# Kernel tuning notes

Measured on AMD Instinct MI355X. Metric: run time of the kernel, lower is better.

The kernel has to match this reference:

```python
import jax, jax.numpy as jnp
import numpy as np

N_ITEMS = 100001  # n_items + 1 (padding idx 0)
D = 128           # item_embedding_dim == hidden_size
P = 3             # purposes
S, B = 100, 256   # seq_len, batch
TAU = 0.1
EPS = 0.01


def setup_inputs() -> dict:
    key = jax.random.key(0)
    ks = jax.random.split(key, 6)
    std = 1.0 / np.sqrt(D)
    seq = jax.random.randint(ks[0], (S, B), 0, N_ITEMS)          # [S, B] item ids
    lens = jax.random.randint(ks[1], (B,), 1, S + 1)             # valid lengths in [1, S]
    emb_table = jax.random.uniform(ks[2], (N_ITEMS, D), minval=-std, maxval=std, dtype=jnp.float32)
    purpose_table = jax.random.uniform(ks[3], (P, D), minval=-std, maxval=std, dtype=jnp.float32)
    x2h_w = jax.random.uniform(ks[4], (P, 3 * D, D), minval=-std, maxval=std, dtype=jnp.float32)  # 3 cells
    h2h_w = jax.random.uniform(ks[5], (P, 3 * D, D), minval=-std, maxval=std, dtype=jnp.float32)
    return {"seq": seq, "lens": lens, "emb_table": emb_table,
            "purpose_table": purpose_table, "x2h_w": x2h_w, "h2h_w": h2h_w}


def _psru_cell(x, h, concen, Wx, Wh):
    # x: [B,D], h: [B,D], concen: [B], Wx/Wh: [3D, D]
    gx = x @ Wx.T                              # [B, 3D]
    gh = h @ Wh.T                              # [B, 3D]
    i_r, i_i, i_n = jnp.split(gx, 3, axis=1)
    h_r, h_i, h_n = jnp.split(gh, 3, axis=1)
    resetgate = jax.nn.sigmoid(i_r + h_r)
    inputgate = jax.nn.sigmoid(i_i + h_i)
    newgate = jnp.tanh(i_n + resetgate * h_n)
    multi = jnp.where(concen >= EPS, concen, 0.0)[:, None] * inputgate
    return h + multi * (newgate - h)


def reference(seq, lens, emb_table, purpose_table, x2h_w, h2h_w):
    # padding_idx = 0
    emb_table = emb_table.at[0].set(0.0)
    # concentration matrix: softmax over purposes of normalized-embedding similarity / tau
    item_n = emb_table / jnp.clip(jnp.linalg.norm(emb_table, axis=1, keepdims=True), 1e-12)
    attr_n = purpose_table / jnp.clip(jnp.linalg.norm(purpose_table, axis=1, keepdims=True), 1e-12)
    g = jax.nn.softmax((item_n @ attr_n.T) / TAU, axis=1)   # [V, P]  (exp/sum == softmax)
    g = g.at[0].set(0.0)

    embs = emb_table[seq]        # [S, B, D]
    g_seq = g[seq]               # [S, B, P]

    h0 = jnp.zeros((P, B, D), emb_table.dtype)

    def step(h, xs):
        x, gq = xs  # x: [B,D], gq: [B,P]
        h_new = jnp.stack([_psru_cell(x, h[p], gq[:, p], x2h_w[p], h2h_w[p]) for p in range(P)])
        return h_new, h_new

    _, hs = jax.lax.scan(step, h0, (embs, g_seq))            # hs: [S, P, B, D]

    # select hidden at last valid step per example: outs[lens-1, arange(B)]
    h_last = hs[lens - 1, :, jnp.arange(B), :]               # [B, P, D]

    # delta_c[b,v] = sum_p g[v,p] * <h_last[b,p], item_n[v]>  (== original VC_cand * item_embs sum)
    logits = sum((h_last[:, p, :] @ item_n.T) * g[None, :, p] for p in range(P))  # [B, V]
    return jax.nn.sigmoid(logits)
```

## Files before the change

### kernel.cpp

```cpp
#include <hip/hip_runtime.h>
#include <hip/hip_bf16.h>
#include <math.h>

#define N_ITEMS 100001
#define DIM 128
#define NP 3
#define SEQ 100
#define NB 256
#define G3 384
#define TAU 0.1f
#define EPS_C 0.01f

#define OFF_G     0
#define OFF_C     300016
#define OFF_WXT   600032
#define OFF_WHT   747488
#define OFF_HLAST 894944
#define OFF_GX    993248
#define WS_FLOATS_PATHA (993248 + 29491200)

typedef float f32x4 __attribute__((ext_vector_type(4)));
typedef short s16x8 __attribute__((ext_vector_type(8)));
typedef unsigned int u32x4 __attribute__((ext_vector_type(4)));
typedef _Float16 f16x8 __attribute__((ext_vector_type(8)));
typedef __fp16 hf16x2 __attribute__((ext_vector_type(2)));

__device__ __forceinline__ float sigmoidf_fast(float x) {
    return __builtin_amdgcn_rcpf(1.f + __builtin_amdgcn_exp2f(-1.4426950408889634f * x));
}
__device__ __forceinline__ float tanhf_fast(float x) {
    return 1.f - 2.f * __builtin_amdgcn_rcpf(1.f + __builtin_amdgcn_exp2f(2.8853900817779268f * x));
}
__device__ __forceinline__ unsigned short f2bf(float x) {
    union { float f; unsigned u; } v; v.f = x;
    unsigned r = v.u + 0x7fffu + ((v.u >> 16) & 1u);
    return (unsigned short)(r >> 16);
}
__device__ __forceinline__ float bf2f(unsigned short h) {
    union { unsigned u; float f; } v; v.u = ((unsigned)h) << 16;
    return v.f;
}
__device__ __forceinline__ f32x4 mfma16(s16x8 a, s16x8 b, f32x4 c) {
    return __builtin_amdgcn_mfma_f32_16x16x32_f16(
        __builtin_bit_cast(f16x8, a), __builtin_bit_cast(f16x8, b), c, 0, 0, 0);
}

__global__ void k_prep_w(const float* __restrict__ x2h, const float* __restrict__ h2h,
                         float* __restrict__ wxT, float* __restrict__ whT) {
    int idx = blockIdx.x * 256 + threadIdx.x;
    if (idx >= NP * DIM * G3) return;
    int j = idx % G3;
    int k = (idx / G3) % DIM;
    int p = idx / (G3 * DIM);
    wxT[idx] = x2h[((size_t)p * G3 + j) * DIM + k];
    whT[idx] = h2h[((size_t)p * G3 + j) * DIM + k];
}

__global__ __launch_bounds__(256) void k_prep_wA(const float* __restrict__ x2h,
                                                 const float* __restrict__ h2h,
                                                 short* __restrict__ wxA_hi,
                                                 short* __restrict__ wxA_lo,
                                                 short* __restrict__ whA_hi,
                                                 short* __restrict__ whA_lo) {
    int e = blockIdx.x * 256 + threadIdx.x;
    if (e >= 2 * NP * 24 * 4 * 64) return;
    int which = (e >= NP * 24 * 4 * 64);
    int f = which ? e - NP * 24 * 4 * 64 : e;
    const float* tab = which ? h2h : x2h;
    short* dh = which ? whA_hi : wxA_hi;
    short* dl = which ? whA_lo : wxA_lo;
    int lane = f & 63;
    int ks = (f >> 6) & 3;
    int mt = (f >> 8) % 24;
    int p  = f / 6144;
    int j = mt * 16 + (lane & 15);
    int d = ks * 32 + (lane >> 4) * 8;
    const float* src = tab + ((size_t)p * G3 + j) * DIM + d;
    short hi[8], lo[8];
#pragma unroll
    for (int u = 0; u < 8; ++u) {
        float x = src[u];
        _Float16 hf = (_Float16)x;
        _Float16 lf = (_Float16)((x - (float)hf) * 2048.f);
        hi[u] = __builtin_bit_cast(short, hf);
        lo[u] = __builtin_bit_cast(short, lf);
    }
    *(s16x8*)(dh + (size_t)f * 8) = *(const s16x8*)hi;
    *(s16x8*)(dl + (size_t)f * 8) = *(const s16x8*)lo;
}

__global__ __launch_bounds__(256) void k_gc(const float* __restrict__ emb,
                                            const float* __restrict__ pt,
                                            float* __restrict__ g, float* __restrict__ c) {
    __shared__ float pt_l[G3];
    __shared__ float ainv[NP];
    int tid = threadIdx.x;
    for (int u = tid; u < G3; u += 256) pt_l[u] = pt[u];
    __syncthreads();
    if (tid < NP) {
        float ss = 0.f;
        for (int k = 0; k < DIM; ++k) { float v = pt_l[tid * DIM + k]; ss += v * v; }
        ainv[tid] = 1.f / fmaxf(sqrtf(ss), 1e-12f);
    }
    __syncthreads();
    int lane = tid & 63, wv = tid >> 6;
    for (int it = 0; it < 8; ++it) {
        int i = blockIdx.x * 32 + wv * 8 + it;
        if (i >= N_ITEMS) continue;
        float a = emb[(size_t)i * DIM + lane];
        float b = emb[(size_t)i * DIM + 64 + lane];
        float ss = a * a + b * b;
        float d0 = a * pt_l[lane]       + b * pt_l[64 + lane];
        float d1 = a * pt_l[128 + lane] + b * pt_l[192 + lane];
        float d2 = a * pt_l[256 + lane] + b * pt_l[320 + lane];
        for (int off = 32; off > 0; off >>= 1) {
            ss += __shfl_down(ss, off);
            d0 += __shfl_down(d0, off);
            d1 += __shfl_down(d1, off);
            d2 += __shfl_down(d2, off);
        }
        if (lane == 0) {
            if (i == 0) {
                g[0] = 0.f; g[1] = 0.f; g[2] = 0.f;
                c[0] = 0.f; c[1] = 0.f; c[2] = 0.f;
            } else {
                float inv = 1.f / fmaxf(sqrtf(ss), 1e-12f);
                float l0 = d0 * ainv[0] * inv * (1.f / TAU);
                float l1 = d1 * ainv[1] * inv * (1.f / TAU);
                float l2 = d2 * ainv[2] * inv * (1.f / TAU);
                float m = fmaxf(l0, fmaxf(l1, l2));
                float e0 = expf(l0 - m), e1 = expf(l1 - m), e2 = expf(l2 - m);
                float is = 1.f / (e0 + e1 + e2);
                float g0 = e0 * is, g1 = e1 * is, g2 = e2 * is;
                g[(size_t)i * 3 + 0] = g0; g[(size_t)i * 3 + 1] = g1; g[(size_t)i * 3 + 2] = g2;
                c[(size_t)i * 3 + 0] = g0 * inv; c[(size_t)i * 3 + 1] = g1 * inv; c[(size_t)i * 3 + 2] = g2 * inv;
            }
        }
    }
}

__global__ __launch_bounds__(512, 2) void k_gx_mfma(const int* __restrict__ seq,
                                                    const float* __restrict__ emb,
                                                    const short* __restrict__ wxA,
                                                    float* __restrict__ gx) {
    int bid = blockIdx.x;
    int t  = bid >> 4;
    int b0 = (bid & 15) * 16;
    int tid = threadIdx.x;
    int lane = tid & 63;
    int w = tid >> 6;
    int n = lane & 15;
    int q = lane >> 4;

    __shared__ int idx_l[16];
    __shared__ __align__(16) unsigned short xF[2048];

    if (tid < 16) idx_l[tid] = seq[t * NB + b0 + tid];
    __syncthreads();

    {
        int tk = tid >> 5, s = tid & 31;
        float4 v = *(const float4*)(emb + (size_t)idx_l[tk] * DIM + s * 4);
        int k = s * 4;
        int ks = k >> 5, km = k & 31;
        int ln = (km >> 3) * 16 + tk;
        int j0 = km & 7;
        int o = ks * 512 + ln * 8 + j0;
        hf16x2 a01 = __builtin_amdgcn_cvt_pkrtz(v.x, v.y);
        hf16x2 a23 = __builtin_amdgcn_cvt_pkrtz(v.z, v.w);
        *(uint2*)(xF + o) = make_uint2(__builtin_bit_cast(unsigned, a01),
                                       __builtin_bit_cast(unsigned, a23));
    }
    __syncthreads();

    s16x8 bf[4];
#pragma unroll
    for (int ks = 0; ks < 4; ++ks)
        bf[ks] = ((const s16x8*)xF)[ks * 64 + lane];

    float* gxt = gx + (size_t)(t * 3) * NB * G3;
#pragma unroll 3
    for (int ji = 0; ji < 9; ++ji) {
        int pid = w + ji * 8;
        int p = pid / 24, mt = pid % 24;
        f32x4 acc = {0.f, 0.f, 0.f, 0.f};
#pragma unroll
        for (int ks = 0; ks < 4; ++ks) {
            size_t ao = ((((size_t)p * 24 + mt) * 4 + ks) * 64 + lane) * 8;
            s16x8 af = *(const s16x8*)(wxA + ao);
            acc = mfma16(af, bf[ks], acc);
        }
        float* o = gxt + ((size_t)p * NB + b0 + n) * G3 + mt * 16 + q * 4;
        *(float4*)o = make_float4(acc[0], acc[1], acc[2], acc[3]);
    }
}

__global__ __launch_bounds__(1024, 4) void k_rnn3(const int* __restrict__ seq,
                                                  const int* __restrict__ lens,
                                                  const float* __restrict__ g,
                                                  const short* __restrict__ whA_hi,
                                                  const float* __restrict__ gx,
                                                  float* __restrict__ hlast) {
    int bid = blockIdx.x;
    int p  = bid / 8;
    int bg = bid % 8;
    int tid = threadIdx.x;
    int tile2 = tid >> 9;
    int tl  = tid & 511;
    int lane = tid & 63;
    int w = tl >> 6;
    int n = lane & 15;
    int q = lane >> 4;
    int d0 = w * 16 + q * 4;
    int b0 = bg * 32 + tile2 * 16;

    __shared__ __align__(16) unsigned short hH[2 * 4096];
    __shared__ __align__(16) unsigned short hL[2 * 4096];
    __shared__ float conc_s[SEQ * 32];

    for (int u = tid; u < 4096; u += 1024) { hH[u] = 0; hL[u] = 0; }

    for (int e = tid; e < SEQ * 32; e += 1024) {
        int t = e >> 5, b = e & 31;
        int ix = seq[t * NB + bg * 32 + b];
        float cc = g[(size_t)ix * 3 + p];
        conc_s[e] = (cc >= EPS_C) ? cc : 0.f;
    }

    s16x8 whF[3][4];
    int mts0 = w, mts1 = 8 + w, mts2 = 16 + w;
#pragma unroll
    for (int ks = 0; ks < 4; ++ks) {
        size_t o0 = ((((size_t)p * 24 + mts0) * 4 + ks) * 64 + lane) * 8;
        size_t o1 = ((((size_t)p * 24 + mts1) * 4 + ks) * 64 + lane) * 8;
        size_t o2 = ((((size_t)p * 24 + mts2) * 4 + ks) * 64 + lane) * 8;
        whF[0][ks] = *(const s16x8*)(whA_hi + o0);
        whF[1][ks] = *(const s16x8*)(whA_hi + o1);
        whF[2][ks] = *(const s16x8*)(whA_hi + o2);
    }

    int len_n = lens[b0 + n];
    float h0 = 0.f, h1 = 0.f, h2 = 0.f, h3 = 0.f;

    int wks = d0 >> 5;
    int km  = d0 & 31;
    int rl  = (km >> 3) * 16 + n;
    int jj0 = km & 7;
    int widx = wks * 512 + rl * 8 + jj0;

    const float* gxbase = gx + ((size_t)p * NB + (b0 + n)) * G3 + d0;
    const size_t tstride = (size_t)3 * NB * G3;

    f32x4 pgr = *(const f32x4*)(gxbase);
    f32x4 pgi = *(const f32x4*)(gxbase + DIM);
    f32x4 pgn = *(const f32x4*)(gxbase + 2 * DIM);

    __syncthreads();

    const float SC = 4.8828125e-4f;

    int cur = 0;
    for (int t = 0; t < SEQ; ++t) {
        f32x4 grv = pgr, giv = pgi, gnv = pgn;
        int tn = (t + 1 < SEQ) ? (t + 1) : t;
        const float* gp = gxbase + (size_t)tn * tstride;
        pgr = *(const f32x4*)(gp);
        pgi = *(const f32x4*)(gp + DIM);
        pgn = *(const f32x4*)(gp + 2 * DIM);

        float cc = conc_s[t * 32 + tile2 * 16 + n];

        const s16x8* bhp = (const s16x8*)hH + cur * 512 + tile2 * 256 + lane;
        const s16x8* blp = (const s16x8*)hL + cur * 512 + tile2 * 256 + lane;
        s16x8 bh0 = bhp[0],   bh1 = bhp[64],  bh2 = bhp[128], bh3 = bhp[192];
        s16x8 bl0 = blp[0],   bl1 = blp[64],  bl2 = blp[128], bl3 = blp[192];

        f32x4 aA0 = grv, aB0 = {0.f,0.f,0.f,0.f};
        aA0 = mfma16(whF[0][0], bh0, aA0);  aB0 = mfma16(whF[0][0], bl0, aB0);
        aA0 = mfma16(whF[0][1], bh1, aA0);  aB0 = mfma16(whF[0][1], bl1, aB0);
        aA0 = mfma16(whF[0][2], bh2, aA0);  aB0 = mfma16(whF[0][2], bl2, aB0);
        aA0 = mfma16(whF[0][3], bh3, aA0);  aB0 = mfma16(whF[0][3], bl3, aB0);
        __builtin_amdgcn_sched_barrier(0);
        float rr0 = sigmoidf_fast(fmaf(aB0[0], SC, aA0[0]));
        float rr1 = sigmoidf_fast(fmaf(aB0[1], SC, aA0[1]));
        float rr2 = sigmoidf_fast(fmaf(aB0[2], SC, aA0[2]));
        float rr3 = sigmoidf_fast(fmaf(aB0[3], SC, aA0[3]));
        __builtin_amdgcn_sched_barrier(0);
        f32x4 aA1 = giv, aB1 = {0.f,0.f,0.f,0.f};
        aA1 = mfma16(whF[1][0], bh0, aA1);  aB1 = mfma16(whF[1][0], bl0, aB1);
        aA1 = mfma16(whF[1][1], bh1, aA1);  aB1 = mfma16(whF[1][1], bl1, aB1);
        aA1 = mfma16(whF[1][2], bh2, aA1);  aB1 = mfma16(whF[1][2], bl2, aB1);
        aA1 = mfma16(whF[1][3], bh3, aA1);  aB1 = mfma16(whF[1][3], bl3, aB1);
        __builtin_amdgcn_sched_barrier(0);
        float m20 = cc * sigmoidf_fast(fmaf(aB1[0], SC, aA1[0]));
        float m21 = cc * sigmoidf_fast(fmaf(aB1[1], SC, aA1[1]));
        float m22 = cc * sigmoidf_fast(fmaf(aB1[2], SC, aA1[2]));
        float m23 = cc * sigmoidf_fast(fmaf(aB1[3], SC, aA1[3]));
        __builtin_amdgcn_sched_barrier(0);
        f32x4 aA2 = {0.f,0.f,0.f,0.f}, aB2 = {0.f,0.f,0.f,0.f};
        aA2 = mfma16(whF[2][0], bh0, aA2);  aB2 = mfma16(whF[2][0], bl0, aB2);
        aA2 = mfma16(whF[2][1], bh1, aA2);  aB2 = mfma16(whF[2][1], bl1, aB2);
        aA2 = mfma16(whF[2][2], bh2, aA2);  aB2 = mfma16(whF[2][2], bl2, aB2);
        aA2 = mfma16(whF[2][3], bh3, aA2);  aB2 = mfma16(whF[2][3], bl3, aB2);
        __builtin_amdgcn_sched_barrier(0);
        float hn0 = fmaf(aB2[0], SC, aA2[0]);
        float hn1 = fmaf(aB2[1], SC, aA2[1]);
        float hn2 = fmaf(aB2[2], SC, aA2[2]);
        float hn3 = fmaf(aB2[3], SC, aA2[3]);
        float ng0 = tanhf_fast(fmaf(rr0, hn0, gnv[0]));
        float ng1 = tanhf_fast(fmaf(rr1, hn1, gnv[1]));
        float ng2 = tanhf_fast(fmaf(rr2, hn2, gnv[2]));
        float ng3 = tanhf_fast(fmaf(rr3, hn3, gnv[3]));
        float hnew0 = fmaf(m20, ng0 - h0, h0);
        float hnew1 = fmaf(m21, ng1 - h1, h1);
        float hnew2 = fmaf(m22, ng2 - h2, h2);
        float hnew3 = fmaf(m23, ng3 - h3, h3);
        h0 = hnew0; h1 = hnew1; h2 = hnew2; h3 = hnew3;

        if (t == len_n - 1) {
            float* hp = hlast + (size_t)(b0 + n) * G3 + p * DIM + d0;
            *(float4*)hp = make_float4(h0, h1, h2, h3);
        }

        hf16x2 c01 = __builtin_amdgcn_cvt_pkrtz(hnew0, hnew1);
        hf16x2 c23 = __builtin_amdgcn_cvt_pkrtz(hnew2, hnew3);
        float e0 = (hnew0 - (float)c01[0]) * 2048.f;
        float e1 = (hnew1 - (float)c01[1]) * 2048.f;
        float e2 = (hnew2 - (float)c23[0]) * 2048.f;
        float e3 = (hnew3 - (float)c23[1]) * 2048.f;
        hf16x2 d01 = __builtin_amdgcn_cvt_pkrtz(e0, e1);
        hf16x2 d23 = __builtin_amdgcn_cvt_pkrtz(e2, e3);
        int wb = (cur ^ 1) * 4096 + tile2 * 2048 + widx;
        *(uint2*)(hH + wb) = make_uint2(__builtin_bit_cast(unsigned, c01),
                                        __builtin_bit_cast(unsigned, c23));
        *(uint2*)(hL + wb) = make_uint2(__builtin_bit_cast(unsigned, d01),
                                        __builtin_bit_cast(unsigned, d23));

        asm volatile("s_waitcnt lgkmcnt(0)" ::: "memory");
        __builtin_amdgcn_sched_barrier(0);
        __builtin_amdgcn_s_barrier();
        __builtin_amdgcn_sched_barrier(0);
        cur ^= 1;
    }
}

__global__ __launch_bounds__(384) void k_rnn(const int* __restrict__ seq,
                                             const int* __restrict__ lens,
                                             const float* __restrict__ emb,
                                             const float* __restrict__ g,
                                             const float* __restrict__ wxT,
                                             const float* __restrict__ whT,
                                             float* __restrict__ hlast) {
    int bid = blockIdx.x;
    int b0 = (bid & 63) * 4;
    int p = bid >> 6;
    __shared__ __align__(16) float h_l[DIM * 4];
    __shared__ __align__(16) float x_l[DIM * 4];
    __shared__ __align__(16) float sx_l[G3 * 4];
    __shared__ __align__(16) float sh_l[G3 * 4];
    __shared__ float conc_l[4];
    __shared__ int idx_l[4];
    __shared__ int len_l[4];
    int tid = threadIdx.x;
    if (tid < 4) len_l[tid] = lens[b0 + tid];
    for (int u = tid; u < DIM * 4; u += 384) h_l[u] = 0.f;
    __syncthreads();
    const float* wh = whT + (size_t)p * (DIM * G3);
    const float* wx = wxT + (size_t)p * (DIM * G3);
    for (int t = 0; t < SEQ; ++t) {
        if (tid < 4) {
            int ix = seq[t * NB + b0 + tid];
            idx_l[tid] = ix;
            conc_l[tid] = g[(size_t)ix * 3 + p];
        }
        __syncthreads();
        for (int u = tid; u < DIM * 4; u += 384) {
            int bc = u >> 7, k = u & 127;
            x_l[k * 4 + bc] = emb[(size_t)idx_l[bc] * DIM + k];
        }
        __syncthreads();
        int j = tid;
        float ax0 = 0.f, ax1 = 0.f, ax2 = 0.f, ax3 = 0.f;
#pragma unroll 4
        for (int k = 0; k < DIM; ++k) {
            float wv = wx[(size_t)k * G3 + j];
            float4 xv = *(const float4*)(x_l + k * 4);
            ax0 += wv * xv.x; ax1 += wv * xv.y; ax2 += wv * xv.z; ax3 += wv * xv.w;
        }
        float ah0 = 0.f, ah1 = 0.f, ah2 = 0.f, ah3 = 0.f;
#pragma unroll 4
        for (int k = 0; k < DIM; ++k) {
            float wv = wh[(size_t)k * G3 + j];
            float4 hv = *(const float4*)(h_l + k * 4);
            ah0 += wv * hv.x; ah1 += wv * hv.y; ah2 += wv * hv.z; ah3 += wv * hv.w;
        }
        *(float4*)(sx_l + j * 4) = make_float4(ax0, ax1, ax2, ax3);
        *(float4*)(sh_l + j * 4) = make_float4(ah0, ah1, ah2, ah3);
        __syncthreads();
        for (int u = tid; u < DIM * 4; u += 384) {
            int bc = u & 3, d = u >> 2;
            float sr = sx_l[d * 4 + bc] + sh_l[d * 4 + bc];
            float si = sx_l[(DIM + d) * 4 + bc] + sh_l[(DIM + d) * 4 + bc];
            float xn = sx_l[(2 * DIM + d) * 4 + bc];
            float hn = sh_l[(2 * DIM + d) * 4 + bc];
            float r  = sigmoidf_fast(sr);
            float ig = sigmoidf_fast(si);
            float ng = tanhf_fast(xn + r * hn);
            float h  = h_l[d * 4 + bc];
            float cc = conc_l[bc];
            float multi = (cc >= EPS_C ? cc : 0.f) * ig;
            float hnew = h + multi * (ng - h);
            h_l[d * 4 + bc] = hnew;
            if (t == len_l[bc] - 1)
                hlast[(size_t)(b0 + bc) * G3 + p * DIM + d] = hnew;
        }
        __syncthreads();
    }
}

__global__ __launch_bounds__(256) void k_prep_h(const float* __restrict__ hlast,
                                                short* __restrict__ hl_hi) {
    int e = blockIdx.x * 256 + threadIdx.x;
    int b = e / G3;
    int k = e % G3;
    float x = hlast[e];
    _Float16 hf = (_Float16)x;
    int off = (k >> 5) * 8192 + b * 32 + ((k >> 3) & 3) * 8 + (k & 7);
    hl_hi[off] = __builtin_bit_cast(short, hf);
}

__global__ __launch_bounds__(256) void k_logits_mfma(const float* __restrict__ emb,
                                                     const float* __restrict__ c,
                                                     const short* __restrict__ hl_hi,
                                                     float* __restrict__ out) {
    int i0 = blockIdx.x * 64;
    int tid = threadIdx.x;
    int w = tid >> 6;
    int lane = tid & 63;
    int n = lane & 15;
    int q = lane >> 4;

    __shared__ __align__(16) float embs[64 * 132];

    for (int u = tid; u < 64 * 32; u += 256) {
        int i = u >> 5;
        int s = u & 31;
        int gi = i0 + i;
        float4 v = make_float4(0.f, 0.f, 0.f, 0.f);
        if (gi < N_ITEMS) v = *(const float4*)(emb + (size_t)gi * DIM + s * 4);
        *(float4*)(embs + i * 132 + s * 4) = v;
    }

    float cv[4][3];
#pragma unroll
    for (int is = 0; is < 4; ++is) {
        int gi = i0 + is * 16 + n;
#pragma unroll
        for (int p = 0; p < 3; ++p)
            cv[is][p] = (gi < N_ITEMS) ? c[(size_t)gi * 3 + p] : 0.f;
    }
    __syncthreads();

    f32x4 acc[4][4];
#pragma unroll
    for (int bs = 0; bs < 4; ++bs)
#pragma unroll
        for (int is = 0; is < 4; ++is)
            acc[bs][is] = (f32x4){0.f, 0.f, 0.f, 0.f};

    for (int ks = 0; ks < 12; ++ks) {
        int p = ks >> 2;
        int d0 = (ks & 3) * 32;
        int abase = ks * 8192 + (w * 64 + n) * 32 + q * 8;
        s16x8 ah[4];
#pragma unroll
        for (int bs = 0; bs < 4; ++bs)
            ah[bs] = *(const s16x8*)(hl_hi + abase + bs * 512);
#pragma unroll
        for (int is = 0; is < 4; ++is) {
            const float* src = embs + (is * 16 + n) * 132 + d0 + q * 8;
            float x[8];
            *(float4*)(x)     = *(const float4*)(src);
            *(float4*)(x + 4) = *(const float4*)(src + 4);
            float sc = cv[is][p];
            union { hf16x2 h[4]; s16x8 s; } bf_;
#pragma unroll
            for (int jp = 0; jp < 4; ++jp)
                bf_.h[jp] = __builtin_amdgcn_cvt_pkrtz(x[2 * jp] * sc, x[2 * jp + 1] * sc);
            s16x8 bv = bf_.s;
#pragma unroll
            for (int bs = 0; bs < 4; ++bs)
                acc[bs][is] = mfma16(ah[bs], bv, acc[bs][is]);
        }
    }

#pragma unroll
    for (int is = 0; is < 4; ++is) {
        int gi = i0 + is * 16 + n;
        if (gi >= N_ITEMS) continue;
#pragma unroll
        for (int bs = 0; bs < 4; ++bs) {
            int brow = w * 64 + bs * 16 + q * 4;
#pragma unroll
            for (int r = 0; r < 4; ++r)
                out[(size_t)(brow + r) * N_ITEMS + gi] = sigmoidf_fast(acc[bs][is][r]);
        }
    }
}

extern "C" void kernel_launch(void* const* d_in, const int* in_sizes, int n_in,
                              void* d_out, int out_size, void* d_ws, size_t ws_size,
                              hipStream_t stream) {
    const int*   seq  = (const int*)d_in[0];
    const int*   lens = (const int*)d_in[1];
    const float* emb  = (const float*)d_in[2];
    const float* pt   = (const float*)d_in[3];
    const float* x2h  = (const float*)d_in[4];
    const float* h2h  = (const float*)d_in[5];
    float* out = (float*)d_out;
    float* ws  = (float*)d_ws;

    float* g     = ws + OFF_G;
    float* c     = ws + OFF_C;
    float* wxT   = ws + OFF_WXT;
    float* whT   = ws + OFF_WHT;
    float* hlast = ws + OFF_HLAST;
    float* gxbuf = ws + OFF_GX;
    short* wxA_hi = (short*)(ws + OFF_WXT);
    short* wxA_lo = wxA_hi + 147456;
    short* whA_hi = (short*)(ws + OFF_WHT);
    short* whA_lo = whA_hi + 147456;
    short* hl_hi = (short*)(ws + OFF_GX);

    int useGx = (ws_size >= (size_t)WS_FLOATS_PATHA * 4) ? 1 : 0;

    k_gc<<<3126, 256, 0, stream>>>(emb, pt, g, c);
    if (useGx) {
        k_prep_wA<<<144, 256, 0, stream>>>(x2h, h2h, wxA_hi, wxA_lo, whA_hi, whA_lo);
        k_gx_mfma<<<1600, 512, 0, stream>>>(seq, emb, wxA_hi, gxbuf);
        k_rnn3<<<24, 1024, 0, stream>>>(seq, lens, g, whA_hi, gxbuf, hlast);
    } else {
        k_prep_w<<<576, 256, 0, stream>>>(x2h, h2h, wxT, whT);
        k_rnn<<<192, 384, 0, stream>>>(seq, lens, emb, g, wxT, whT, hlast);
    }
    k_prep_h<<<384, 256, 0, stream>>>(hlast, hl_hi);
    k_logits_mfma<<<1563, 256, 0, stream>>>(emb, c, hl_hi, out);
}
```

Baseline: 427.0 us.

## Drop fp16 hi/lo split for hidden state and halve RNN block size

The recurrent kernel now keeps the hidden state in shared memory as a single fp16 value instead of an fp16 high part plus a scaled low-residual part. This halves the MFMA count and the shared-memory traffic per timestep. It also splits the work into 48 blocks of 512 threads, each handling 16 batch rows, instead of 24 blocks of 1024 threads, so the per-step barrier spans fewer waves. The cost is lower precision in the recurrence, since the hidden state loses about 11 bits of mantissa at each step and the error can accumulate over 100 steps.

Measured after the change: 361.8 us. 15.3% less time.

```diff
diff --git a/kernel.cpp b/kernel.cpp
--- a/kernel.cpp
+++ b/kernel.cpp
@@ -195,34 +195,30 @@
     }
 }
 
-__global__ __launch_bounds__(1024, 4) void k_rnn3(const int* __restrict__ seq,
-                                                  const int* __restrict__ lens,
-                                                  const float* __restrict__ g,
-                                                  const short* __restrict__ whA_hi,
-                                                  const float* __restrict__ gx,
-                                                  float* __restrict__ hlast) {
+__global__ __launch_bounds__(512, 2) void k_rnn3(const int* __restrict__ seq,
+                                                 const int* __restrict__ lens,
+                                                 const float* __restrict__ g,
+                                                 const short* __restrict__ whA_hi,
+                                                 const float* __restrict__ gx,
+                                                 float* __restrict__ hlast) {
     int bid = blockIdx.x;
-    int p  = bid / 8;
-    int bg = bid % 8;
+    int p  = bid / 16;
+    int b0 = (bid % 16) * 16;
     int tid = threadIdx.x;
-    int tile2 = tid >> 9;
-    int tl  = tid & 511;
     int lane = tid & 63;
-    int w = tl >> 6;
+    int w = tid >> 6;
     int n = lane & 15;
     int q = lane >> 4;
     int d0 = w * 16 + q * 4;
-    int b0 = bg * 32 + tile2 * 16;
-
-    __shared__ __align__(16) unsigned short hH[2 * 4096];
-    __shared__ __align__(16) unsigned short hL[2 * 4096];
-    __shared__ float conc_s[SEQ * 32];
-
-    for (int u = tid; u < 4096; u += 1024) { hH[u] = 0; hL[u] = 0; }
-
-    for (int e = tid; e < SEQ * 32; e += 1024) {
-        int t = e >> 5, b = e & 31;
-        int ix = seq[t * NB + bg * 32 + b];
+
+    __shared__ __align__(16) unsigned short hH[2 * 2048];
+    __shared__ float conc_s[SEQ * 16];
+
+    for (int u = tid; u < 2048; u += 512) hH[u] = 0;
+
+    for (int e = tid; e < SEQ * 16; e += 512) {
+        int t = e >> 4, b = e & 15;
+        int ix = seq[t * NB + b0 + b];
         float cc = g[(size_t)ix * 3 + p];
         conc_s[e] = (cc >= EPS_C) ? cc : 0.f;
     }
@@ -256,8 +252,6 @@
     f32x4 pgn = *(const f32x4*)(gxbase + 2 * DIM);
 
     __syncthreads();
-
-    const float SC = 4.8828125e-4f;
 
     int cur = 0;
     for (int t = 0; t < SEQ; ++t) {
@@ -268,49 +262,43 @@
         pgi = *(const f32x4*)(gp + DIM);
         pgn = *(const f32x4*)(gp + 2 * DIM);
 
-        float cc = conc_s[t * 32 + tile2 * 16 + n];
-
-        const s16x8* bhp = (const s16x8*)hH + cur * 512 + tile2 * 256 + lane;
-        const s16x8* blp = (const s16x8*)hL + cur * 512 + tile2 * 256 + lane;
-        s16x8 bh0 = bhp[0],   bh1 = bhp[64],  bh2 = bhp[128], bh3 = bhp[192];
-        s16x8 bl0 = blp[0],   bl1 = blp[64],  bl2 = blp[128], bl3 = blp[192];
-
-        f32x4 aA0 = grv, aB0 = {0.f,0.f,0.f,0.f};
-        aA0 = mfma16(whF[0][0], bh0, aA0);  aB0 = mfma16(whF[0][0], bl0, aB0);
-        aA0 = mfma16(whF[0][1], bh1, aA0);  aB0 = mfma16(whF[0][1], bl1, aB0);
-        aA0 = mfma16(whF[0][2], bh2, aA0);  aB0 = mfma16(whF[0][2], bl2, aB0);
-        aA0 = mfma16(whF[0][3], bh3, aA0);  aB0 = mfma16(whF[0][3], bl3, aB0);
-        __builtin_amdgcn_sched_barrier(0);
-        float rr0 = sigmoidf_fast(fmaf(aB0[0], SC, aA0[0]));
-        float rr1 = sigmoidf_fast(fmaf(aB0[1], SC, aA0[1]));
-        float rr2 = sigmoidf_fast(fmaf(aB0[2], SC, aA0[2]));
-        float rr3 = sigmoidf_fast(fmaf(aB0[3], SC, aA0[3]));
-        __builtin_amdgcn_sched_barrier(0);
-        f32x4 aA1 = giv, aB1 = {0.f,0.f,0.f,0.f};
-        aA1 = mfma16(whF[1][0], bh0, aA1);  aB1 = mfma16(whF[1][0], bl0, aB1);
-        aA1 = mfma16(whF[1][1], bh1, aA1);  aB1 = mfma16(whF[1][1], bl1, aB1);
-        aA1 = mfma16(whF[1][2], bh2, aA1);  aB1 = mfma16(whF[1][2], bl2, aB1);
-        aA1 = mfma16(whF[1][3], bh3, aA1);  aB1 = mfma16(whF[1][3], bl3, aB1);
-        __builtin_amdgcn_sched_barrier(0);
-        float m20 = cc * sigmoidf_fast(fmaf(aB1[0], SC, aA1[0]));
-        float m21 = cc * sigmoidf_fast(fmaf(aB1[1], SC, aA1[1]));
-        float m22 = cc * sigmoidf_fast(fmaf(aB1[2], SC, aA1[2]));
-        float m23 = cc * sigmoidf_fast(fmaf(aB1[3], SC, aA1[3]));
-        __builtin_amdgcn_sched_barrier(0);
-        f32x4 aA2 = {0.f,0.f,0.f,0.f}, aB2 = {0.f,0.f,0.f,0.f};
-        aA2 = mfma16(whF[2][0], bh0, aA2);  aB2 = mfma16(whF[2][0], bl0, aB2);
-        aA2 = mfma16(whF[2][1], bh1, aA2);  aB2 = mfma16(whF[2][1], bl1, aB2);
-        aA2 = mfma16(whF[2][2], bh2, aA2);  aB2 = mfma16(whF[2][2], bl2, aB2);
-        aA2 = mfma16(whF[2][3], bh3, aA2);  aB2 = mfma16(whF[2][3], bl3, aB2);
-        __builtin_amdgcn_sched_barrier(0);
-        float hn0 = fmaf(aB2[0], SC, aA2[0]);
-        float hn1 = fmaf(aB2[1], SC, aA2[1]);
-        float hn2 = fmaf(aB2[2], SC, aA2[2]);
-        float hn3 = fmaf(aB2[3], SC, aA2[3]);
-        float ng0 = tanhf_fast(fmaf(rr0, hn0, gnv[0]));
-        float ng1 = tanhf_fast(fmaf(rr1, hn1, gnv[1]));
-        float ng2 = tanhf_fast(fmaf(rr2, hn2, gnv[2]));
-        float ng3 = tanhf_fast(fmaf(rr3, hn3, gnv[3]));
+        float cc = conc_s[t * 16 + n];
+
+        const s16x8* bhp = (const s16x8*)hH + cur * 256 + lane;
+        s16x8 bh0 = bhp[0], bh1 = bhp[64], bh2 = bhp[128], bh3 = bhp[192];
+
+        f32x4 aA0 = grv;
+        aA0 = mfma16(whF[0][0], bh0, aA0);
+        aA0 = mfma16(whF[0][1], bh1, aA0);
+        aA0 = mfma16(whF[0][2], bh2, aA0);
+        aA0 = mfma16(whF[0][3], bh3, aA0);
+        __builtin_amdgcn_sched_barrier(0);
+        float rr0 = sigmoidf_fast(aA0[0]);
+        float rr1 = sigmoidf_fast(aA0[1]);
+        float rr2 = sigmoidf_fast(aA0[2]);
+        float rr3 = sigmoidf_fast(aA0[3]);
+        __builtin_amdgcn_sched_barrier(0);
+        f32x4 aA1 = giv;
+        aA1 = mfma16(whF[1][0], bh0, aA1);
+        aA1 = mfma16(whF[1][1], bh1, aA1);
+        aA1 = mfma16(whF[1][2], bh2, aA1);
+        aA1 = mfma16(whF[1][3], bh3, aA1);
+        __builtin_amdgcn_sched_barrier(0);
+        float m20 = cc * sigmoidf_fast(aA1[0]);
+        float m21 = cc * sigmoidf_fast(aA1[1]);
+        float m22 = cc * sigmoidf_fast(aA1[2]);
+        float m23 = cc * sigmoidf_fast(aA1[3]);
+        __builtin_amdgcn_sched_barrier(0);
+        f32x4 aA2 = {0.f,0.f,0.f,0.f};
+        aA2 = mfma16(whF[2][0], bh0, aA2);
+        aA2 = mfma16(whF[2][1], bh1, aA2);
+        aA2 = mfma16(whF[2][2], bh2, aA2);
+        aA2 = mfma16(whF[2][3], bh3, aA2);
+        __builtin_amdgcn_sched_barrier(0);
+        float ng0 = tanhf_fast(fmaf(rr0, aA2[0], gnv[0]));
+        float ng1 = tanhf_fast(fmaf(rr1, aA2[1], gnv[1]));
+        float ng2 = tanhf_fast(fmaf(rr2, aA2[2], gnv[2]));
+        float ng3 = tanhf_fast(fmaf(rr3, aA2[3], gnv[3]));
         float hnew0 = fmaf(m20, ng0 - h0, h0);
         float hnew1 = fmaf(m21, ng1 - h1, h1);
         float hnew2 = fmaf(m22, ng2 - h2, h2);
@@ -324,17 +312,9 @@
 
         hf16x2 c01 = __builtin_amdgcn_cvt_pkrtz(hnew0, hnew1);
         hf16x2 c23 = __builtin_amdgcn_cvt_pkrtz(hnew2, hnew3);
-        float e0 = (hnew0 - (float)c01[0]) * 2048.f;
-        float e1 = (hnew1 - (float)c01[1]) * 2048.f;
-        float e2 = (hnew2 - (float)c23[0]) * 2048.f;
-        float e3 = (hnew3 - (float)c23[1]) * 2048.f;
-        hf16x2 d01 = __builtin_amdgcn_cvt_pkrtz(e0, e1);
-        hf16x2 d23 = __builtin_amdgcn_cvt_pkrtz(e2, e3);
-        int wb = (cur ^ 1) * 4096 + tile2 * 2048 + widx;
+        int wb = (cur ^ 1) * 2048 + widx;
         *(uint2*)(hH + wb) = make_uint2(__builtin_bit_cast(unsigned, c01),
                                         __builtin_bit_cast(unsigned, c23));
-        *(uint2*)(hL + wb) = make_uint2(__builtin_bit_cast(unsigned, d01),
-                                        __builtin_bit_cast(unsigned, d23));
 
         asm volatile("s_waitcnt lgkmcnt(0)" ::: "memory");
         __builtin_amdgcn_sched_barrier(0);
@@ -538,7 +518,7 @@
     if (useGx) {
         k_prep_wA<<<144, 256, 0, stream>>>(x2h, h2h, wxA_hi, wxA_lo, whA_hi, whA_lo);
         k_gx_mfma<<<1600, 512, 0, stream>>>(seq, emb, wxA_hi, gxbuf);
-        k_rnn3<<<24, 1024, 0, stream>>>(seq, lens, g, whA_hi, gxbuf, hlast);
+        k_rnn3<<<48, 512, 0, stream>>>(seq, lens, g, whA_hi, gxbuf, hlast);
     } else {
         k_prep_w<<<576, 256, 0, stream>>>(x2h, h2h, wxT, whT);
         k_rnn<<<192, 384, 0, stream>>>(seq, lens, emb, g, wxT, whT, hlast);
```
